# Kernel optimization log

Measured on AMD Instinct MI355X. Metric: run time of the kernel, lower is better.

The kernel has to match this reference:

```python
import jax, jax.numpy as jnp
import numpy as np

N_NODES = 100000
N_EDGES = 3200000
N_GRAPHS = 125  # 800 nodes per graph
D_IN, D_H1, D_H2, D_OUT = 64, 64, 64, 64


def setup_inputs() -> dict:
    key = jax.random.key(0)
    ks = jax.random.split(key, 9)
    x = jax.random.normal(ks[0], (N_NODES, D_IN), dtype=jnp.float32)
    edge_index = jax.random.randint(ks[1], (2, N_EDGES), 0, N_NODES, dtype=jnp.int32)
    ptr = jnp.arange(0, N_NODES + 1, N_NODES // N_GRAPHS, dtype=jnp.int32)  # [126]
    s1 = 1.0 / np.sqrt(D_IN)
    s2 = 1.0 / np.sqrt(D_H1)
    s3 = 1.0 / np.sqrt(D_H2)
    W1 = jax.random.normal(ks[2], (D_IN, D_H1), jnp.float32) * s1
    b1 = jnp.zeros((D_H1,), jnp.float32)
    W2 = jax.random.normal(ks[3], (D_H1, D_H2), jnp.float32) * s2
    b2 = jnp.zeros((D_H2,), jnp.float32)
    Wf = jax.random.normal(ks[4], (D_H2, D_OUT), jnp.float32) * s3
    bf = jax.random.normal(ks[5], (D_OUT,), jnp.float32) * s3
    return {"x": x, "edge_index": edge_index, "ptr": ptr,
            "W1": W1, "b1": b1, "W2": W2, "b2": b2, "Wf": Wf, "bf": bf}


def _gcn_conv(x, src, dst, deg_inv_sqrt, W, b):
    # PyG GCNConv: h = x @ W; symmetric norm with self-loops; scatter-add; + bias
    h = x @ W                                    # [N, d_out]
    norm = deg_inv_sqrt[src] * deg_inv_sqrt[dst]  # [E]
    msg = h[src] * norm[:, None]                 # [E, d_out] gather + scale
    agg = jax.ops.segment_sum(msg, dst, num_segments=N_NODES)
    # self-loop contribution: norm_ii = deg_inv_sqrt[i]^2
    agg = agg + h * (deg_inv_sqrt ** 2)[:, None]
    return agg + b


def reference(x, edge_index, ptr, W1, b1, W2, b2, Wf, bf):
    src = edge_index[0]
    dst = edge_index[1]
    # degree at target, including the self-loop
    deg = jax.ops.segment_sum(jnp.ones((N_EDGES,), x.dtype), dst,
                              num_segments=N_NODES) + 1.0
    deg_inv_sqrt = jax.lax.rsqrt(deg)

    h = jax.nn.relu(_gcn_conv(x, src, dst, deg_inv_sqrt, W1, b1))
    h = jax.nn.relu(_gcn_conv(h, src, dst, deg_inv_sqrt, W2, b2))
    h = h @ Wf + bf                              # [N, D_OUT]

    # mean aggregation per graph defined by ptr boundaries
    seg = jnp.searchsorted(ptr, jnp.arange(N_NODES, dtype=ptr.dtype),
                           side='right') - 1     # [N] graph id per node
    sums = jax.ops.segment_sum(h, seg, num_segments=N_GRAPHS)  # [G, D_OUT]
    counts = (ptr[1:] - ptr[:-1]).astype(h.dtype)              # [G]
    return sums / counts[:, None]
```

## Files before the change

kernel.cpp:

```cpp
#include <hip/hip_runtime.h>
#include <hip/hip_bf16.h>

#define N_NODES 100000
#define N_EDGES 3200000
#define N_GRAPHS 125
#define D 64
#define NB 800
#define BW 125
#define CAP 5120
#define SC_WGS 512
#define SC_EPW 6250
#define SC_THREADS 1024
#define SC_ITERS 7
#define BUILD_THREADS 512
#define BUILD_ITERS 10

typedef __bf16 bf16x8 __attribute__((ext_vector_type(8)));
typedef float f32x4 __attribute__((ext_vector_type(4)));
typedef float f32x2 __attribute__((ext_vector_type(2)));

__device__ __forceinline__ float bf_lo(unsigned u) { return __uint_as_float(u << 16); }
__device__ __forceinline__ float bf_hi(unsigned u) { return __uint_as_float(u & 0xffff0000u); }
__device__ __forceinline__ f32x2 bf2(unsigned u) {
    f32x2 r;
    r.x = __uint_as_float(u << 16);
    r.y = __uint_as_float(u & 0xffff0000u);
    return r;
}
__device__ __forceinline__ unsigned short f2bf(float f) {
    unsigned u = __float_as_uint(f);
    return (unsigned short)((u + 0x7fffu + ((u >> 16) & 1u)) >> 16);
}


__global__ void bucket_scatter(const int* __restrict__ src, const int* __restrict__ dst,
                               int* __restrict__ bcursor, unsigned* __restrict__ pairs) {
    __shared__ unsigned stage[SC_EPW];
    __shared__ unsigned short bkt[SC_EPW];
    __shared__ int hist[NB];
    __shared__ int cursor[NB];
    __shared__ int goff[NB];
    __shared__ int wsum[16];
    int wg = blockIdx.x, t = threadIdx.x;
    int e0 = wg * SC_EPW;
    if (t < NB) hist[t] = 0;
    __syncthreads();
    unsigned pw[SC_ITERS];
    int      bl[SC_ITERS];
#pragma unroll
    for (int j = 0; j < SC_ITERS; ++j) {
        int o = t + j * SC_THREADS;
        if (o < SC_EPW) {
            int i = e0 + o;
            int s = src[i], d = dst[i];
            int b = d / BW;
            pw[j] = ((unsigned)s << 7) | (unsigned)(d - b * BW);
            bl[j] = b;
            atomicAdd(&hist[b], 1);
        }
    }
    __syncthreads();
    int own = (t < NB) ? hist[t] : 0;
    int incl = own;
#pragma unroll
    for (int off = 1; off < 64; off <<= 1) {
        int v = __shfl_up(incl, off);
        if ((t & 63) >= off) incl += v;
    }
    if ((t & 63) == 63) wsum[t >> 6] = incl;
    __syncthreads();
    if (t < 16) {
        int v = wsum[t];
#pragma unroll
        for (int off = 1; off < 16; off <<= 1) {
            int u = __shfl_up(v, off);
            if (t >= off) v += u;
        }
        wsum[t] = v;
    }
    __syncthreads();
    if (t < NB) {
        int wb = (t >> 6) ? wsum[(t >> 6) - 1] : 0;
        int lstart = wb + incl - own;
        cursor[t] = lstart;
        int gbase = t * CAP + (own ? atomicAdd(&bcursor[t], own) : 0);
        goff[t] = gbase - lstart;
    }
    __syncthreads();
#pragma unroll
    for (int j = 0; j < SC_ITERS; ++j) {
        int o = t + j * SC_THREADS;
        if (o < SC_EPW) {
            int pos = atomicAdd(&cursor[bl[j]], 1);
            stage[pos] = pw[j];
            bkt[pos] = (unsigned short)bl[j];
        }
    }
    __syncthreads();
#pragma unroll
    for (int j = 0; j < SC_ITERS; ++j) {
        int i = t + j * SC_THREADS;
        if (i < SC_EPW) {
            int b = bkt[i];
            pairs[goff[b] + i] = stage[i];
        }
    }
}

__global__ void bucket_build(const unsigned* __restrict__ pairs, const int* __restrict__ bcursor,
                             int* __restrict__ deg, float* __restrict__ dis,
                             int* __restrict__ row_start, int* __restrict__ csr) {
    __shared__ int h8[8][128];
    __shared__ int cur8[8][128];
    __shared__ int sc[128];
    int b = blockIdx.x, t = threadIdx.x;
    int w = t >> 6;
    int nb = b * BW;
    for (int i = t; i < 8 * 128; i += BUILD_THREADS) ((int*)h8)[i] = 0;
    __syncthreads();
    int base = b * CAP, n = bcursor[b];
    unsigned pw[BUILD_ITERS];
#pragma unroll
    for (int j = 0; j < BUILD_ITERS; ++j) {
        int i = t + j * BUILD_THREADS;
        if (i < n) {
            unsigned p = pairs[base + i];
            pw[j] = p;
            atomicAdd(&h8[w][p & 127u], 1);
        }
    }
    __syncthreads();
    int own = 0, own_pad = 0;
    if (t < 128) {
        int s = 0;
#pragma unroll
        for (int ww = 0; ww < 8; ++ww) {
            cur8[ww][t] = s;
            s += h8[ww][t];
        }
        own = (t < BW) ? s : 0;
        own_pad = (own + 7) & ~7;
        sc[t] = own_pad;
    }
    if (t < BW) {
        deg[nb + t] = own;
        dis[nb + t] = rsqrtf((float)own + 1.0f);
    }
    __syncthreads();
    for (int off = 1; off < 128; off <<= 1) {
        int v = (t >= off && t < 128) ? sc[t - off] : 0;
        __syncthreads();
        if (t < 128) sc[t] += v;
        __syncthreads();
    }
    if (t < 128) {
        int rs = base + sc[t] - own_pad;
        if (t < BW) {
            row_start[nb + t] = rs;
            for (int k = own; k < own_pad; ++k)
                csr[rs + k] = N_NODES;
        }
#pragma unroll
        for (int ww = 0; ww < 8; ++ww)
            cur8[ww][t] += rs;
    }
    __syncthreads();
#pragma unroll
    for (int j = 0; j < BUILD_ITERS; ++j) {
        int i = t + j * BUILD_THREADS;
        if (i < n) {
            unsigned p = pw[j];
            int pos = atomicAdd(&cur8[w][p & 127u], 1);
            csr[pos] = (int)(p >> 7);
        }
    }
}


__global__ void mfma_gemm(const unsigned short* __restrict__ Xb, const float* __restrict__ W,
                          const float* __restrict__ dis, unsigned short* __restrict__ Y) {
    int lane = threadIdx.x & 63;
    int wid  = (blockIdx.x * blockDim.x + threadIdx.x) >> 6;
    int nwav = (gridDim.x * blockDim.x) >> 6;
    int nl = lane & 15;
    int kq = lane >> 4;
    int kb = kq * 8;
    union BV { unsigned short s[8]; bf16x8 v; } b0[4], b1[4];
#pragma unroll
    for (int nt = 0; nt < 4; ++nt) {
        int nn = nt * 16 + nl;
#pragma unroll
        for (int j = 0; j < 8; ++j) {
            b0[nt].s[j] = f2bf(W[(kb + j) * 64 + nn]);
            b1[nt].s[j] = f2bf(W[(32 + kb + j) * 64 + nn]);
        }
    }
    const uint4* X4 = (const uint4*)Xb;
    for (int t = wid; t < N_NODES / 16; t += nwav) {
        int m0 = t * 16;
        uint4 a0u = X4[(size_t)(m0 + nl) * 8 + kq];
        uint4 a1u = X4[(size_t)(m0 + nl) * 8 + 4 + kq];
        bf16x8 a0 = __builtin_bit_cast(bf16x8, a0u);
        bf16x8 a1 = __builtin_bit_cast(bf16x8, a1u);
        f32x4 acc[4];
#pragma unroll
        for (int nt = 0; nt < 4; ++nt) {
            acc[nt] = (f32x4){0.0f, 0.0f, 0.0f, 0.0f};
            acc[nt] = __builtin_amdgcn_mfma_f32_16x16x32_bf16(a0, b0[nt].v, acc[nt], 0, 0, 0);
            acc[nt] = __builtin_amdgcn_mfma_f32_16x16x32_bf16(a1, b1[nt].v, acc[nt], 0, 0, 0);
        }
        int rbase = m0 + kq * 4;
        float d0 = dis[rbase], d1 = dis[rbase + 1], d2 = dis[rbase + 2], d3 = dis[rbase + 3];
#pragma unroll
        for (int nt = 0; nt < 4; ++nt) {
            int nn = nt * 16 + nl;
            Y[(size_t)(rbase + 0) * 64 + nn] = f2bf(acc[nt][0] * d0);
            Y[(size_t)(rbase + 1) * 64 + nn] = f2bf(acc[nt][1] * d1);
            Y[(size_t)(rbase + 2) * 64 + nn] = f2bf(acc[nt][2] * d2);
            Y[(size_t)(rbase + 3) * 64 + nn] = f2bf(acc[nt][3] * d3);
        }
    }
}

__global__ void mfma_gemm_f32(const float* __restrict__ X, const float* __restrict__ W,
                              const float* __restrict__ dis, unsigned short* __restrict__ Y) {
    int lane = threadIdx.x & 63;
    int wid  = (blockIdx.x * blockDim.x + threadIdx.x) >> 6;
    int nwav = (gridDim.x * blockDim.x) >> 6;
    int nl = lane & 15;
    int kq = lane >> 4;
    int kb = kq * 8;
    union BV { unsigned short s[8]; bf16x8 v; } b0[4], b1[4];
#pragma unroll
    for (int nt = 0; nt < 4; ++nt) {
        int nn = nt * 16 + nl;
#pragma unroll
        for (int j = 0; j < 8; ++j) {
            b0[nt].s[j] = f2bf(W[(kb + j) * 64 + nn]);
            b1[nt].s[j] = f2bf(W[(32 + kb + j) * 64 + nn]);
        }
    }
    const float4* Xf = (const float4*)X;
    for (int t = wid; t < N_NODES / 16; t += nwav) {
        int m0 = t * 16;
        size_t rb = (size_t)(m0 + nl) * 16;
        float4 f0 = Xf[rb + 2 * kq];
        float4 f1 = Xf[rb + 2 * kq + 1];
        float4 f2 = Xf[rb + 8 + 2 * kq];
        float4 f3 = Xf[rb + 8 + 2 * kq + 1];
        union BV av0, av1;
        av0.s[0] = f2bf(f0.x); av0.s[1] = f2bf(f0.y); av0.s[2] = f2bf(f0.z); av0.s[3] = f2bf(f0.w);
        av0.s[4] = f2bf(f1.x); av0.s[5] = f2bf(f1.y); av0.s[6] = f2bf(f1.z); av0.s[7] = f2bf(f1.w);
        av1.s[0] = f2bf(f2.x); av1.s[1] = f2bf(f2.y); av1.s[2] = f2bf(f2.z); av1.s[3] = f2bf(f2.w);
        av1.s[4] = f2bf(f3.x); av1.s[5] = f2bf(f3.y); av1.s[6] = f2bf(f3.z); av1.s[7] = f2bf(f3.w);
        f32x4 acc[4];
#pragma unroll
        for (int nt = 0; nt < 4; ++nt) {
            acc[nt] = (f32x4){0.0f, 0.0f, 0.0f, 0.0f};
            acc[nt] = __builtin_amdgcn_mfma_f32_16x16x32_bf16(av0.v, b0[nt].v, acc[nt], 0, 0, 0);
            acc[nt] = __builtin_amdgcn_mfma_f32_16x16x32_bf16(av1.v, b1[nt].v, acc[nt], 0, 0, 0);
        }
        int rbase = m0 + kq * 4;
        float d0 = dis[rbase], d1 = dis[rbase + 1], d2 = dis[rbase + 2], d3 = dis[rbase + 3];
#pragma unroll
        for (int nt = 0; nt < 4; ++nt) {
            int nn = nt * 16 + nl;
            Y[(size_t)(rbase + 0) * 64 + nn] = f2bf(acc[nt][0] * d0);
            Y[(size_t)(rbase + 1) * 64 + nn] = f2bf(acc[nt][1] * d1);
            Y[(size_t)(rbase + 2) * 64 + nn] = f2bf(acc[nt][2] * d2);
            Y[(size_t)(rbase + 3) * 64 + nn] = f2bf(acc[nt][3] * d3);
        }
    }
}

__global__ void gather_kernel(const unsigned short* __restrict__ Hb, const int* __restrict__ csr,
                              const int* __restrict__ row_start, const int* __restrict__ deg,
                              const float* __restrict__ dis,
                              const float* __restrict__ bias, void* __restrict__ Out,
                              int do_relu, int fuse_pool, float* __restrict__ P) {
    __shared__ float tmp[4][64];
    int v    = (blockIdx.x * blockDim.x + threadIdx.x) >> 6;
    int lane = threadIdx.x & 63;
    int oct  = lane >> 3;
    int l8   = lane & 7;
    int base = row_start[v];
    int n = deg[v];
    float disv = dis[v];
    const uint4* H4 = (const uint4*)Hb;

    f32x2 c0 = {0.f, 0.f}, c1 = {0.f, 0.f}, c2 = {0.f, 0.f}, c3 = {0.f, 0.f};
    if (oct == 0) {
        uint4 hv = H4[((unsigned)v << 3) + (unsigned)l8];
        c0 = bf2(hv.x); c1 = bf2(hv.y); c2 = bf2(hv.z); c3 = bf2(hv.w);
    }

    int groups = (n + 7) >> 3;
    const int* cp = csr + base + oct;
#pragma unroll 4
    for (int g = 0; g < groups; ++g) {
        int ssrc = cp[g << 3];
        uint4 hv = H4[((unsigned)ssrc << 3) + (unsigned)l8];
        c0 += bf2(hv.x); c1 += bf2(hv.y);
        c2 += bf2(hv.z); c3 += bf2(hv.w);
    }
    float a0 = c0.x, a1 = c0.y, a2 = c1.x, a3 = c1.y;
    float a4 = c2.x, a5 = c2.y, a6 = c3.x, a7 = c3.y;
#pragma unroll
    for (int off = 8; off <= 32; off <<= 1) {
        a0 += __shfl_xor(a0, off); a1 += __shfl_xor(a1, off);
        a2 += __shfl_xor(a2, off); a3 += __shfl_xor(a3, off);
        a4 += __shfl_xor(a4, off); a5 += __shfl_xor(a5, off);
        a6 += __shfl_xor(a6, off); a7 += __shfl_xor(a7, off);
    }
    if (oct == 0) {
        float4 blo = ((const float4*)bias)[2 * l8];
        float4 bhi = ((const float4*)bias)[2 * l8 + 1];
        a0 = fmaf(a0, disv, blo.x); a1 = fmaf(a1, disv, blo.y);
        a2 = fmaf(a2, disv, blo.z); a3 = fmaf(a3, disv, blo.w);
        a4 = fmaf(a4, disv, bhi.x); a5 = fmaf(a5, disv, bhi.y);
        a6 = fmaf(a6, disv, bhi.z); a7 = fmaf(a7, disv, bhi.w);
        if (do_relu) {
            a0 = fmaxf(a0, 0.0f); a1 = fmaxf(a1, 0.0f); a2 = fmaxf(a2, 0.0f); a3 = fmaxf(a3, 0.0f);
            a4 = fmaxf(a4, 0.0f); a5 = fmaxf(a5, 0.0f); a6 = fmaxf(a6, 0.0f); a7 = fmaxf(a7, 0.0f);
        }
        if (!fuse_pool) {
            union { unsigned short s[8]; uint4 u; } p;
            p.s[0] = f2bf(a0); p.s[1] = f2bf(a1); p.s[2] = f2bf(a2); p.s[3] = f2bf(a3);
            p.s[4] = f2bf(a4); p.s[5] = f2bf(a5); p.s[6] = f2bf(a6); p.s[7] = f2bf(a7);
            ((uint4*)Out)[((unsigned)v << 3) + (unsigned)l8] = p.u;
        } else {
            float* tr = &tmp[threadIdx.x >> 6][l8 * 8];
            tr[0] = a0; tr[1] = a1; tr[2] = a2; tr[3] = a3;
            tr[4] = a4; tr[5] = a5; tr[6] = a6; tr[7] = a7;
        }
    }
    if (fuse_pool) {
        __syncthreads();
        if (threadIdx.x < 64) {
            int cc = threadIdx.x;
            float s = tmp[0][cc] + tmp[1][cc] + tmp[2][cc] + tmp[3][cc];
            int g = blockIdx.x / 200;
            atomicAdd(&P[g * 64 + cc], s);
        }
    }
}

__global__ void gemm_kernel(const float* __restrict__ X, const float* __restrict__ W,
                            const float* __restrict__ bias, float* __restrict__ Y,
                            int nrows) {
    __shared__ float Ws[64][64];
    for (int i = threadIdx.x; i < 64 * 64; i += 256)
        Ws[i >> 6][i & 63] = W[i];
    __syncthreads();
    int c  = threadIdx.x & 63;
    int rl = threadIdx.x >> 6;
    int r  = blockIdx.x * 4 + rl;
    if (r < nrows) {
        const float* xr = X + (size_t)r * D;
        float dot = 0.0f;
#pragma unroll
        for (int k = 0; k < 64; ++k)
            dot = fmaf(xr[k], Ws[k][c], dot);
        Y[(size_t)r * D + c] = fmaf(dot, 1.0f / 800.0f, bias[c]);
    }
}

extern "C" void kernel_launch(void* const* d_in, const int* in_sizes, int n_in,
                              void* d_out, int out_size, void* d_ws, size_t ws_size,
                              hipStream_t stream) {
    const float* x   = (const float*)d_in[0];
    const int*   ei  = (const int*)d_in[1];
    const int*   src = ei;
    const int*   dst = ei + N_EDGES;
    const float* W1  = (const float*)d_in[3];
    const float* b1  = (const float*)d_in[4];
    const float* W2  = (const float*)d_in[5];
    const float* b2  = (const float*)d_in[6];
    const float* Wf  = (const float*)d_in[7];
    const float* bfp = (const float*)d_in[8];
    float* out = (float*)d_out;

    int*   deg       = (int*)d_ws;
    int*   row_start = deg + 100352;
    int*   bcursor   = row_start + 100352;
    float* P         = (float*)(bcursor + 1024);
    float* dis       = P + 8192;
    int*   csr       = (int*)(dis + 100352);
    float* R         = (float*)(csr + 4096000);
    unsigned short* Ab = (unsigned short*)R;
    unsigned short* Hb = (unsigned short*)(R + 3200064);
    unsigned* pairs  = (unsigned*)(R + 6400128);

    hipMemsetAsync(bcursor, 0, (1024 + 8192) * sizeof(int), stream);
    hipMemsetAsync(Ab + (size_t)N_NODES * D, 0, D * sizeof(unsigned short), stream);
    bucket_scatter<<<SC_WGS, SC_THREADS, 0, stream>>>(src, dst, bcursor, pairs);
    bucket_build<<<NB, BUILD_THREADS, 0, stream>>>(pairs, bcursor, deg, dis, row_start, csr);

    const int grid4 = (N_NODES + 3) / 4;

    mfma_gemm_f32<<<782, 256, 0, stream>>>(x, W1, dis, Ab);
    gather_kernel<<<grid4, 256, 0, stream>>>(Ab, csr, row_start, deg, dis, b1, Hb, 1, 0, nullptr);

    mfma_gemm<<<782, 256, 0, stream>>>(Hb, W2, dis, Ab);
    gather_kernel<<<grid4, 256, 0, stream>>>(Ab, csr, row_start, deg, dis, b2, nullptr, 1, 1, P);

    gemm_kernel<<<(N_GRAPHS + 3) / 4, 256, 0, stream>>>(P, Wf, bfp, out, N_GRAPHS);
}
```

Baseline: 272.8 us.

## Fold memsets into bucket kernels, vectorize edge loads, use wave-level scan in build

Removes one memset and shrinks the other by zeroing the Ab sentinel row inside bucket_scatter and the P accumulator inside bucket_build. bucket_scatter now runs 500 workgroups of 6400 edges and reads src/dst as int4 vectors, four edges per thread. bucket_build swaps its barrier-heavy shared-memory prefix scan for a wavefront shuffle scan with a single cross-wave fixup. The aim is fewer launches and barriers and wider loads, at the cost of more registers per thread in scatter.

```diff
diff --git a/kernel.cpp b/kernel.cpp
--- a/kernel.cpp
+++ b/kernel.cpp
@@ -8,10 +8,11 @@
 #define NB 800
 #define BW 125
 #define CAP 5120
-#define SC_WGS 512
-#define SC_EPW 6250
+#define SC_WGS 500
+#define SC_EPW 6400
 #define SC_THREADS 1024
-#define SC_ITERS 7
+#define SC_G4 1600
+#define SC_WITERS 7
 #define BUILD_THREADS 512
 #define BUILD_ITERS 10
 
@@ -34,7 +35,8 @@
 
 
 __global__ void bucket_scatter(const int* __restrict__ src, const int* __restrict__ dst,
-                               int* __restrict__ bcursor, unsigned* __restrict__ pairs) {
+                               int* __restrict__ bcursor, unsigned* __restrict__ pairs,
+                               unsigned short* __restrict__ Ab_sentinel) {
     __shared__ unsigned stage[SC_EPW];
     __shared__ unsigned short bkt[SC_EPW];
     __shared__ int hist[NB];
@@ -42,21 +44,26 @@
     __shared__ int goff[NB];
     __shared__ int wsum[16];
     int wg = blockIdx.x, t = threadIdx.x;
-    int e0 = wg * SC_EPW;
+    if (wg == 0 && t < 8) {
+        uint4 z = {0u, 0u, 0u, 0u};
+        ((uint4*)Ab_sentinel)[t] = z;
+    }
     if (t < NB) hist[t] = 0;
     __syncthreads();
-    unsigned pw[SC_ITERS];
-    int      bl[SC_ITERS];
-#pragma unroll
-    for (int j = 0; j < SC_ITERS; ++j) {
-        int o = t + j * SC_THREADS;
-        if (o < SC_EPW) {
-            int i = e0 + o;
-            int s = src[i], d = dst[i];
-            int b = d / BW;
-            pw[j] = ((unsigned)s << 7) | (unsigned)(d - b * BW);
-            bl[j] = b;
-            atomicAdd(&hist[b], 1);
+    const int4* s4p = (const int4*)src + (size_t)wg * SC_G4;
+    const int4* d4p = (const int4*)dst + (size_t)wg * SC_G4;
+    unsigned pw[8];
+    int      bl[8];
+#pragma unroll
+    for (int j = 0; j < 2; ++j) {
+        int g = t + j * SC_THREADS;
+        if (g < SC_G4) {
+            int4 s4 = s4p[g];
+            int4 d4 = d4p[g];
+            int b0 = d4.x / BW; pw[j*4+0] = ((unsigned)s4.x << 7) | (unsigned)(d4.x - b0*BW); bl[j*4+0] = b0; atomicAdd(&hist[b0], 1);
+            int b1 = d4.y / BW; pw[j*4+1] = ((unsigned)s4.y << 7) | (unsigned)(d4.y - b1*BW); bl[j*4+1] = b1; atomicAdd(&hist[b1], 1);
+            int b2 = d4.z / BW; pw[j*4+2] = ((unsigned)s4.z << 7) | (unsigned)(d4.z - b2*BW); bl[j*4+2] = b2; atomicAdd(&hist[b2], 1);
+            int b3 = d4.w / BW; pw[j*4+3] = ((unsigned)s4.w << 7) | (unsigned)(d4.w - b3*BW); bl[j*4+3] = b3; atomicAdd(&hist[b3], 1);
         }
     }
     __syncthreads();
@@ -88,17 +95,20 @@
     }
     __syncthreads();
 #pragma unroll
-    for (int j = 0; j < SC_ITERS; ++j) {
-        int o = t + j * SC_THREADS;
-        if (o < SC_EPW) {
-            int pos = atomicAdd(&cursor[bl[j]], 1);
-            stage[pos] = pw[j];
-            bkt[pos] = (unsigned short)bl[j];
-        }
-    }
-    __syncthreads();
-#pragma unroll
-    for (int j = 0; j < SC_ITERS; ++j) {
+    for (int j = 0; j < 2; ++j) {
+        int g = t + j * SC_THREADS;
+        if (g < SC_G4) {
+#pragma unroll
+            for (int k = 0; k < 4; ++k) {
+                int pos = atomicAdd(&cursor[bl[j*4+k]], 1);
+                stage[pos] = pw[j*4+k];
+                bkt[pos] = (unsigned short)bl[j*4+k];
+            }
+        }
+    }
+    __syncthreads();
+#pragma unroll
+    for (int j = 0; j < SC_WITERS; ++j) {
         int i = t + j * SC_THREADS;
         if (i < SC_EPW) {
             int b = bkt[i];
@@ -109,13 +119,18 @@
 
 __global__ void bucket_build(const unsigned* __restrict__ pairs, const int* __restrict__ bcursor,
                              int* __restrict__ deg, float* __restrict__ dis,
-                             int* __restrict__ row_start, int* __restrict__ csr) {
+                             int* __restrict__ row_start, int* __restrict__ csr,
+                             float* __restrict__ P) {
     __shared__ int h8[8][128];
     __shared__ int cur8[8][128];
-    __shared__ int sc[128];
+    __shared__ int scv[4];
     int b = blockIdx.x, t = threadIdx.x;
     int w = t >> 6;
     int nb = b * BW;
+    if (b < 8) {
+        P[b * 1024 + t] = 0.0f;
+        P[b * 1024 + 512 + t] = 0.0f;
+    }
     for (int i = t; i < 8 * 128; i += BUILD_THREADS) ((int*)h8)[i] = 0;
     __syncthreads();
     int base = b * CAP, n = bcursor[b];
@@ -140,21 +155,22 @@
         }
         own = (t < BW) ? s : 0;
         own_pad = (own + 7) & ~7;
-        sc[t] = own_pad;
     }
     if (t < BW) {
         deg[nb + t] = own;
         dis[nb + t] = rsqrtf((float)own + 1.0f);
     }
-    __syncthreads();
-    for (int off = 1; off < 128; off <<= 1) {
-        int v = (t >= off && t < 128) ? sc[t - off] : 0;
-        __syncthreads();
-        if (t < 128) sc[t] += v;
-        __syncthreads();
-    }
+    int incl = own_pad;
+#pragma unroll
+    for (int off = 1; off < 64; off <<= 1) {
+        int v = __shfl_up(incl, off);
+        if ((t & 63) >= off) incl += v;
+    }
+    if (t == 63) scv[0] = incl;
+    __syncthreads();
+    if (t >= 64 && t < 128) incl += scv[0];
     if (t < 128) {
-        int rs = base + sc[t] - own_pad;
+        int rs = base + incl - own_pad;
         if (t < BW) {
             row_start[nb + t] = rs;
             for (int k = own; k < own_pad; ++k)
@@ -391,10 +407,10 @@
     unsigned short* Hb = (unsigned short*)(R + 3200064);
     unsigned* pairs  = (unsigned*)(R + 6400128);
 
-    hipMemsetAsync(bcursor, 0, (1024 + 8192) * sizeof(int), stream);
-    hipMemsetAsync(Ab + (size_t)N_NODES * D, 0, D * sizeof(unsigned short), stream);
-    bucket_scatter<<<SC_WGS, SC_THREADS, 0, stream>>>(src, dst, bcursor, pairs);
-    bucket_build<<<NB, BUILD_THREADS, 0, stream>>>(pairs, bcursor, deg, dis, row_start, csr);
+    hipMemsetAsync(bcursor, 0, NB * sizeof(int), stream);
+    bucket_scatter<<<SC_WGS, SC_THREADS, 0, stream>>>(src, dst, bcursor, pairs,
+                                                      Ab + (size_t)N_NODES * D);
+    bucket_build<<<NB, BUILD_THREADS, 0, stream>>>(pairs, bcursor, deg, dis, row_start, csr, P);
 
     const int grid4 = (N_NODES + 3) / 4;
 
```

After: 272.9 us. Within noise of the previous version (+0.0%).
